# Kernel optimization log

Measured on AMD Instinct MI355X. Metric: run time of the kernel, lower is better.

## Reference

```python
import jax, jax.numpy as jnp
import numpy as np

B, SRC_SEQ, SRC_DIMS = 1024, 336, 64
ORDER, TAR_SEQ = 168, 96


def setup_inputs() -> dict:
    key = jax.random.key(0)
    k1, k2 = jax.random.split(key, 2)
    inputs = jax.random.normal(k1, (B, SRC_SEQ, SRC_DIMS), dtype=jnp.float32)
    # Per-channel Dense(order -> tar_seq_len): stacked kernels and biases.
    W = jax.random.normal(k2, (SRC_DIMS, ORDER, TAR_SEQ), dtype=jnp.float32) * (1.0 / np.sqrt(ORDER))
    b = jnp.zeros((SRC_DIMS, TAR_SEQ), dtype=jnp.float32)
    return {"inputs": inputs, "W": W, "b": b, "training": 0}


def reference(inputs, W, b, training):
    # inputs: [B, S, C]; W: [C, order, T]; b: [C, T]
    order = W.shape[1]
    x = jnp.transpose(inputs, (0, 2, 1))[:, :, -order:]  # [B, C, order]
    # Fused per-channel linear projection (batched over channels):
    y = jnp.einsum('bco,cot->bct', x, W) + b             # [B, C, T]
    return jnp.transpose(y, (0, 2, 1))                    # [B, T, C]
```

## Files before the change

### kernel.cpp

```cpp
#include <hip/hip_runtime.h>

#define BATCH 1024
#define SEQ   336
#define CCH   64
#define ORD   168
#define TT    96
#define OFF   168
#define KP    192
#define RSC   25
#define YSTR  9

typedef __attribute__((ext_vector_type(8))) short  short8;
typedef __attribute__((ext_vector_type(8))) unsigned short ushort8;
typedef __attribute__((ext_vector_type(4))) float  floatx4;

#define WT2_ELEMS ((size_t)CCH * 36 * 512)
#define WS_NEED   (WT2_ELEMS * 2)

__device__ __forceinline__ unsigned short f2bf(float f) {
    union { float f; unsigned u; } v; v.f = f;
    unsigned r = v.u + 0x7FFF + ((v.u >> 16) & 1);
    return (unsigned short)(r >> 16);
}

__global__ __launch_bounds__(256)
void k1w(const float* __restrict__ W, unsigned short* __restrict__ Wt2)
{
    const int tid = threadIdx.x, l = tid & 63, w = tid >> 6;
    const int wid = blockIdx.x * 4 + w;
    const int kc = wid % 6;
    const int n  = (wid / 6) % 6;
    const int c  = wid / 36;
    const int m  = l & 15, kg = l >> 4;
    const int t  = n * 16 + m;
    ushort8 u;
    #pragma unroll
    for (int j = 0; j < 8; ++j) {
        int o = kc * 32 + kg * 8 + j;
        float val = (o < ORD) ? W[((size_t)c * ORD + o) * TT + t] : 0.f;
        u[j] = f2bf(val);
    }
    *(ushort8*)(Wt2 + (size_t)wid * 512 + l * 8) = u;
}

__global__ __launch_bounds__(512, 4)
void k2f(const float* __restrict__ inp, const unsigned short* __restrict__ Wt2,
         const float* __restrict__ bias, float* __restrict__ out)
{
    __shared__ float smem_f[16 * TT * YSTR];
    unsigned short* Xs = (unsigned short*)smem_f;

    const int tid = threadIdx.x, l = tid & 63, wv = tid >> 6;
    const int m = l & 15, kg = l >> 4;
    const int btile = (blockIdx.x & 7) | ((blockIdx.x >> 6) << 3);
    const int cg    = (blockIdx.x >> 3) & 7;
    const int b0 = btile * 16, c0 = cg * 8;

    floatx4 f[2][8];
    #pragma unroll
    for (int i = 0; i < 2; ++i) {
        int v = tid + i * 512;
        if (v < 768) {
            int cq = v & 1, b = (v >> 1) & 15, kchunk = v >> 5;
            #pragma unroll
            for (int j = 0; j < 8; ++j) {
                int o = kchunk * 8 + j;
                floatx4 z = {0.f, 0.f, 0.f, 0.f};
                f[i][j] = (o < ORD)
                    ? *(const floatx4*)(inp + ((size_t)(b0 + b) * SEQ + OFF + o) * CCH + c0 + cq * 4)
                    : z;
            }
        }
    }
    #pragma unroll
    for (int i = 0; i < 2; ++i) {
        int v = tid + i * 512;
        if (v < 768) {
            int cq = v & 1, b = (v >> 1) & 15, kchunk = v >> 5;
            #pragma unroll
            for (int cc = 0; cc < 4; ++cc) {
                int c = cq * 4 + cc;
                ushort8 u;
                #pragma unroll
                for (int j = 0; j < 8; ++j) u[j] = f2bf(f[i][j][cc]);
                *(ushort8*)(Xs + (((c * 16 + b) * RSC + (kchunk ^ (c & 7))) << 3)) = u;
            }
        }
    }

    float bv[6];
    #pragma unroll
    for (int n = 0; n < 6; ++n)
        bv[n] = bias[(c0 + wv) * TT + n * 16 + m];

    __syncthreads();

    floatx4 acc[6] = {};
    {
        const int c = wv;
        short8 a[6];
        #pragma unroll
        for (int kc = 0; kc < 6; ++kc) {
            int chunk = (kc * 4 + kg) ^ (c & 7);
            a[kc] = *(const short8*)(Xs + (((c * 16 + m) * RSC + chunk) << 3));
        }
        const unsigned short* Wc = Wt2 + (size_t)(c0 + c) * 36 * 512;
        #pragma unroll
        for (int kc = 0; kc < 6; ++kc) {
            #pragma unroll
            for (int n = 0; n < 6; ++n) {
                short8 bfrag = *(const short8*)(Wc + (size_t)(n * 6 + kc) * 512 + l * 8);
                acc[n] = __builtin_amdgcn_mfma_f32_16x16x32_bf16(a[kc], bfrag, acc[n], 0, 0, 0);
            }
        }
    }

    __syncthreads();

    float* Ys = smem_f;
    {
        const int c = wv;
        #pragma unroll
        for (int n = 0; n < 6; ++n)
            #pragma unroll
            for (int r = 0; r < 4; ++r) {
                int row = kg * 4 + r;
                Ys[(row * TT + n * 16 + m) * YSTR + c] = acc[n][r] + bv[n];
            }
    }
    __syncthreads();
    {
        int c4  = tid & 1;
        int te  = (tid >> 1) & 15;
        int row = tid >> 5;
        #pragma unroll
        for (int s = 0; s < 6; ++s) {
            int tt = te + s * 16;
            floatx4 y = *(const floatx4*)(Ys + (row * TT + tt) * YSTR + c4 * 4);
            *(floatx4*)(out + ((size_t)(b0 + row) * TT + tt) * CCH + c0 + c4 * 4) = y;
        }
    }
}

#define MB  8
#define NT  16
#define KO  8
#define NCH (ORD/KO)
#define WSTRIDE 132
typedef __attribute__((address_space(3))) void* lds_ptr_t;
typedef const __attribute__((address_space(1))) void* gbl_ptr_t;

__global__ __launch_bounds__(256, 4)
void tcl_fallback(const float* __restrict__ inp, const float* __restrict__ W,
                  const float* __restrict__ bias, float* __restrict__ out)
{
    __shared__ float Xsf[MB * KO * CCH];
    __shared__ float Wsf[CCH * WSTRIDE];
    const int tid = threadIdx.x;
    const int c   = tid & 63;
    const int tg  = tid >> 6;
    const int bblk = blockIdx.x & 127;
    const int tblk = blockIdx.x >> 7;
    const int b0 = bblk * MB;
    const int t0 = tblk * NT;
    float acc[MB][4];
    #pragma unroll
    for (int bi = 0; bi < MB; ++bi)
        #pragma unroll
        for (int tj = 0; tj < 4; ++tj) acc[bi][tj] = 0.f;
    for (int ch = 0; ch < NCH; ++ch) {
        const int ob = ch * KO;
        #pragma unroll
        for (int k = 0; k < 4; ++k) {
            int v = tid + k * 256;
            int row = v >> 4, c4 = v & 15;
            int bi = row >> 3, oi = row & 7;
            const float* gp = inp + ((size_t)(b0 + bi) * SEQ + (OFF + ob + oi)) * CCH + c4 * 4;
            __builtin_amdgcn_global_load_lds((gbl_ptr_t)gp, (lds_ptr_t)(Xsf + v * 4), 16, 0, 0);
        }
        float4 wbuf[8];
        #pragma unroll
        for (int k = 0; k < 8; ++k) {
            int v = tid + k * 256;
            int cch = v >> 5, oi = (v >> 2) & 7, t4 = v & 3;
            wbuf[k] = *(const float4*)(W + (size_t)cch * (ORD * TT) + (size_t)(ob + oi) * TT + t0 + t4 * 4);
        }
        #pragma unroll
        for (int k = 0; k < 8; ++k) {
            int v = tid + k * 256;
            int cch = v >> 5, oi = (v >> 2) & 7, t4 = v & 3;
            *(float4*)(Wsf + cch * WSTRIDE + oi * NT + t4 * 4) = wbuf[k];
        }
        __syncthreads();
        #pragma unroll
        for (int oi = 0; oi < KO; ++oi) {
            const float4 wvv = *(const float4*)(Wsf + c * WSTRIDE + oi * NT + tg * 4);
            float xv[MB];
            #pragma unroll
            for (int bi = 0; bi < MB; ++bi) xv[bi] = Xsf[(bi * KO + oi) * CCH + c];
            #pragma unroll
            for (int bi = 0; bi < MB; ++bi) {
                acc[bi][0] += xv[bi] * wvv.x;
                acc[bi][1] += xv[bi] * wvv.y;
                acc[bi][2] += xv[bi] * wvv.z;
                acc[bi][3] += xv[bi] * wvv.w;
            }
        }
        __syncthreads();
    }
    const float4 bvv = *(const float4*)(bias + c * TT + t0 + tg * 4);
    #pragma unroll
    for (int bi = 0; bi < MB; ++bi) {
        size_t base = ((size_t)(b0 + bi) * TT + (t0 + tg * 4)) * CCH + c;
        out[base]           = acc[bi][0] + bvv.x;
        out[base + CCH]     = acc[bi][1] + bvv.y;
        out[base + 2 * CCH] = acc[bi][2] + bvv.z;
        out[base + 3 * CCH] = acc[bi][3] + bvv.w;
    }
}

extern "C" void kernel_launch(void* const* d_in, const int* in_sizes, int n_in,
                              void* d_out, int out_size, void* d_ws, size_t ws_size,
                              hipStream_t stream) {
    const float* inp  = (const float*)d_in[0];
    const float* W    = (const float*)d_in[1];
    const float* bias = (const float*)d_in[2];
    float* out = (float*)d_out;

    if (ws_size >= WS_NEED) {
        unsigned short* Wt2 = (unsigned short*)d_ws;
        k1w<<<576, 256, 0, stream>>>(W, Wt2);
        k2f<<<512, 512, 0, stream>>>(inp, Wt2, bias, out);
    } else {
        tcl_fallback<<<768, 256, 0, stream>>>(inp, W, bias, out);
    }
}
```

Before: 146.7 us.

## Double batch rows per block to reuse W fragments across two MFMA tiles

Each k2f block now covers 32 batch rows instead of 16, so every bf16 W fragment loaded from global memory feeds two MFMAs, one per 16-row half. The grid shrinks from 512 to 256 blocks and uses about 100KB of dynamic LDS, with the occupancy hint lowered to 2. The output is written in two rounds through the transpose buffer, whose padding stride changes from 9 to 12. The aim is to halve W fragment traffic per output, at the cost of fewer, larger blocks, extra barriers and less latency hiding on a memory-bound kernel.

Result: no change. 147.3 us (+0.4%).

```diff
diff --git a/kernel.cpp b/kernel.cpp
--- a/kernel.cpp
+++ b/kernel.cpp
@@ -8,7 +8,7 @@
 #define OFF   168
 #define KP    192
 #define RSC   25
-#define YSTR  9
+#define YSTR  12
 
 typedef __attribute__((ext_vector_type(8))) short  short8;
 typedef __attribute__((ext_vector_type(8))) unsigned short ushort8;
@@ -16,6 +16,7 @@
 
 #define WT2_ELEMS ((size_t)CCH * 36 * 512)
 #define WS_NEED   (WT2_ELEMS * 2)
+#define K2_LDS    (8 * 32 * RSC * 16)
 
 __device__ __forceinline__ unsigned short f2bf(float f) {
     union { float f; unsigned u; } v; v.f = f;
@@ -43,48 +44,39 @@
     *(ushort8*)(Wt2 + (size_t)wid * 512 + l * 8) = u;
 }
 
-__global__ __launch_bounds__(512, 4)
+__global__ __launch_bounds__(512, 2)
 void k2f(const float* __restrict__ inp, const unsigned short* __restrict__ Wt2,
          const float* __restrict__ bias, float* __restrict__ out)
 {
-    __shared__ float smem_f[16 * TT * YSTR];
+    extern __shared__ float smem_f[];
     unsigned short* Xs = (unsigned short*)smem_f;
 
     const int tid = threadIdx.x, l = tid & 63, wv = tid >> 6;
     const int m = l & 15, kg = l >> 4;
     const int btile = (blockIdx.x & 7) | ((blockIdx.x >> 6) << 3);
     const int cg    = (blockIdx.x >> 3) & 7;
-    const int b0 = btile * 16, c0 = cg * 8;
-
-    floatx4 f[2][8];
-    #pragma unroll
-    for (int i = 0; i < 2; ++i) {
+    const int b0 = btile * 32, c0 = cg * 8;
+
+    #pragma unroll
+    for (int i = 0; i < 3; ++i) {
         int v = tid + i * 512;
-        if (v < 768) {
-            int cq = v & 1, b = (v >> 1) & 15, kchunk = v >> 5;
-            #pragma unroll
-            for (int j = 0; j < 8; ++j) {
-                int o = kchunk * 8 + j;
-                floatx4 z = {0.f, 0.f, 0.f, 0.f};
-                f[i][j] = (o < ORD)
-                    ? *(const floatx4*)(inp + ((size_t)(b0 + b) * SEQ + OFF + o) * CCH + c0 + cq * 4)
-                    : z;
-            }
-        }
-    }
-    #pragma unroll
-    for (int i = 0; i < 2; ++i) {
-        int v = tid + i * 512;
-        if (v < 768) {
-            int cq = v & 1, b = (v >> 1) & 15, kchunk = v >> 5;
-            #pragma unroll
-            for (int cc = 0; cc < 4; ++cc) {
-                int c = cq * 4 + cc;
-                ushort8 u;
-                #pragma unroll
-                for (int j = 0; j < 8; ++j) u[j] = f2bf(f[i][j][cc]);
-                *(ushort8*)(Xs + (((c * 16 + b) * RSC + (kchunk ^ (c & 7))) << 3)) = u;
-            }
+        int cq = v & 1, b = (v >> 1) & 31, kchunk = v >> 6;
+        floatx4 f[8];
+        #pragma unroll
+        for (int j = 0; j < 8; ++j) {
+            int o = kchunk * 8 + j;
+            floatx4 z = {0.f, 0.f, 0.f, 0.f};
+            f[j] = (o < ORD)
+                ? *(const floatx4*)(inp + ((size_t)(b0 + b) * SEQ + OFF + o) * CCH + c0 + cq * 4)
+                : z;
+        }
+        #pragma unroll
+        for (int cc = 0; cc < 4; ++cc) {
+            int c = cq * 4 + cc;
+            ushort8 u;
+            #pragma unroll
+            for (int j = 0; j < 8; ++j) u[j] = f2bf(f[j][cc]);
+            *(ushort8*)(Xs + (((c * 32 + b) * RSC + (kchunk ^ (c & 7))) << 3)) = u;
         }
     }
 
@@ -95,22 +87,19 @@
 
     __syncthreads();
 
-    floatx4 acc[6] = {};
+    floatx4 acc0[6] = {}, acc1[6] = {};
     {
-        const int c = wv;
-        short8 a[6];
+        const unsigned short* Wc = Wt2 + (size_t)(c0 + wv) * 36 * 512;
         #pragma unroll
         for (int kc = 0; kc < 6; ++kc) {
-            int chunk = (kc * 4 + kg) ^ (c & 7);
-            a[kc] = *(const short8*)(Xs + (((c * 16 + m) * RSC + chunk) << 3));
-        }
-        const unsigned short* Wc = Wt2 + (size_t)(c0 + c) * 36 * 512;
-        #pragma unroll
-        for (int kc = 0; kc < 6; ++kc) {
+            int chunk = (kc * 4 + kg) ^ (wv & 7);
+            short8 a0 = *(const short8*)(Xs + (((wv * 32 + m)      * RSC + chunk) << 3));
+            short8 a1 = *(const short8*)(Xs + (((wv * 32 + 16 + m) * RSC + chunk) << 3));
             #pragma unroll
             for (int n = 0; n < 6; ++n) {
                 short8 bfrag = *(const short8*)(Wc + (size_t)(n * 6 + kc) * 512 + l * 8);
-                acc[n] = __builtin_amdgcn_mfma_f32_16x16x32_bf16(a[kc], bfrag, acc[n], 0, 0, 0);
+                acc0[n] = __builtin_amdgcn_mfma_f32_16x16x32_bf16(a0, bfrag, acc0[n], 0, 0, 0);
+                acc1[n] = __builtin_amdgcn_mfma_f32_16x16x32_bf16(a1, bfrag, acc1[n], 0, 0, 0);
             }
         }
     }
@@ -118,27 +107,31 @@
     __syncthreads();
 
     float* Ys = smem_f;
-    {
-        const int c = wv;
-        #pragma unroll
-        for (int n = 0; n < 6; ++n)
-            #pragma unroll
-            for (int r = 0; r < 4; ++r) {
-                int row = kg * 4 + r;
-                Ys[(row * TT + n * 16 + m) * YSTR + c] = acc[n][r] + bv[n];
+    #pragma unroll
+    for (int rnd = 0; rnd < 2; ++rnd) {
+        {
+            #pragma unroll
+            for (int n = 0; n < 6; ++n)
+                #pragma unroll
+                for (int r = 0; r < 4; ++r) {
+                    int row = kg * 4 + r;
+                    float val = (rnd == 0 ? acc0[n][r] : acc1[n][r]) + bv[n];
+                    Ys[(row * TT + n * 16 + m) * YSTR + wv] = val;
+                }
+        }
+        __syncthreads();
+        {
+            int c4  = tid & 1;
+            int te  = (tid >> 1) & 15;
+            int row = tid >> 5;
+            #pragma unroll
+            for (int s = 0; s < 6; ++s) {
+                int tt = te + s * 16;
+                floatx4 y = *(const floatx4*)(Ys + (row * TT + tt) * YSTR + c4 * 4);
+                *(floatx4*)(out + ((size_t)(b0 + rnd * 16 + row) * TT + tt) * CCH + c0 + c4 * 4) = y;
             }
-    }
-    __syncthreads();
-    {
-        int c4  = tid & 1;
-        int te  = (tid >> 1) & 15;
-        int row = tid >> 5;
-        #pragma unroll
-        for (int s = 0; s < 6; ++s) {
-            int tt = te + s * 16;
-            floatx4 y = *(const floatx4*)(Ys + (row * TT + tt) * YSTR + c4 * 4);
-            *(floatx4*)(out + ((size_t)(b0 + row) * TT + tt) * CCH + c0 + c4 * 4) = y;
-        }
+        }
+        __syncthreads();
     }
 }
 
@@ -230,7 +223,7 @@
     if (ws_size >= WS_NEED) {
         unsigned short* Wt2 = (unsigned short*)d_ws;
         k1w<<<576, 256, 0, stream>>>(W, Wt2);
-        k2f<<<512, 512, 0, stream>>>(inp, Wt2, bias, out);
+        k2f<<<256, 512, K2_LDS, stream>>>(inp, Wt2, bias, out);
     } else {
         tcl_fallback<<<768, 256, 0, stream>>>(inp, W, bias, out);
     }
```
